# Performance work log

Measured on AMD Instinct MI355X. Metric: run time of the kernel, lower is better.

The kernel has to match this reference:

```python
import jax, jax.numpy as jnp
import numpy as np

FREQ_NUM = 3
MAX_STEP = 4
PERIODS = np.array([24.0, 7.0, 365.0], dtype=np.float32)  # ceil(sups - infs)
INFS = np.array([0.0, 0.0, 0.0], dtype=np.float32)
BS, H, W, L, D = 128, 56, 56, 64, 128
Z_DIM = 3 * H * W + L * D + D            # 17728
EMB_DIM = 2 * FREQ_NUM                   # sin/cos per frequency
IN_DIM = Z_DIM + 2 * EMB_DIM             # 17740
HID = 4096
N_POI, N_USER = 5000, 1000


def setup_inputs() -> dict:
    key = jax.random.key(0)
    ks = jax.random.split(key, 10)
    sups = jnp.asarray(PERIODS)
    return {
        "input_freq": jax.random.uniform(ks[0], (BS, H, W), jnp.float32),
        "input_seq": jax.random.randint(ks[1], (BS, L), 0, N_POI),
        "uid": jax.random.randint(ks[2], (BS,), 0, N_USER),
        "cur_time": jax.random.uniform(ks[3], (BS, FREQ_NUM), jnp.float32) * sups,
        "tar_time": jax.random.uniform(ks[4], (BS, FREQ_NUM), jnp.float32) * sups,
        "fuse_embed": jax.random.normal(ks[5], (N_POI + N_USER, D), jnp.float32),
        "W1": jax.random.normal(ks[6], (IN_DIM, HID), jnp.float32) / np.sqrt(IN_DIM),
        "b1": jnp.zeros((HID,), jnp.float32),
        "W2": jax.random.normal(ks[7], (HID, Z_DIM), jnp.float32) / np.sqrt(HID),
        "b2": jnp.zeros((Z_DIM,), jnp.float32),
        "n_poi": N_POI,
    }


def _time_grid(cur_time, tar_time):
    # Per-sample linspace with periodic wraparound; snapshot t0_ after each
    # micro-step assignment (intended semantics of the torch loop).
    periods = jnp.asarray(PERIODS)
    frac = jnp.linspace(0.0, 1.0, MAX_STEP)  # [4]
    rows = []
    t_cur = cur_time
    for j in range(FREQ_NUM):
        s = cur_time[:, j]
        e = tar_time[:, j]
        wrap = s > e
        e_adj = jnp.where(wrap, e + periods[j], e)
        inter = s[:, None] + (e_adj - s)[:, None] * frac[None, :]  # [bs,4]
        inter = jnp.where(wrap[:, None], jnp.mod(inter, periods[j]), inter)
        for k in range(MAX_STEP):
            t_cur = t_cur.at[:, j].set(inter[:, k])
            rows.append(t_cur)
    return jnp.stack(rows, axis=0)  # [4*freq_num, bs, freq_num]


def _time_embedding(T):
    # sinusoidal embedding per frequency band
    phase = 2.0 * jnp.pi * (T - jnp.asarray(INFS)) / jnp.asarray(PERIODS)
    return jnp.concatenate([jnp.sin(phase), jnp.cos(phase)], axis=-1)  # [S,bs,2F]


def reference(input_freq, input_seq, uid, cur_time, tar_time, fuse_embed,
              W1, b1, W2, b2, n_poi):
    bs = input_freq.shape[0]
    A = jnp.tile(input_freq[:, None], (1, 3, 1, 1)).reshape(bs, -1)     # [bs,3HW]
    x = fuse_embed[input_seq].transpose(0, 2, 1).reshape(bs, -1)        # [bs,D*L]
    u = fuse_embed[n_poi + uid].reshape(bs, -1)                          # [bs,D]
    z0 = jnp.concatenate([A, x, u], axis=-1)                             # [bs,Z_DIM]

    T = _time_grid(cur_time, tar_time)
    emb = _time_embedding(T)                                             # [S,bs,2F]

    def step(z, te):
        t0e, t1e = te
        inp = jnp.concatenate([z, t0e, t1e], axis=-1)
        dz = jnp.tanh(inp @ W1 + b1) @ W2 + b2
        return z + dz, None

    z, _ = jax.lax.scan(step, z0, (emb[:-1], emb[1:]))
    return z
```

## Files before the change

### kernel.cpp

```cpp
#include <hip/hip_runtime.h>
#include <math.h>

typedef __bf16 bf16;
typedef __bf16 bf16x8 __attribute__((ext_vector_type(8)));
typedef float f32x4 __attribute__((ext_vector_type(4)));

#define ZDIM 17728
#define HIDN 4096
#define BSZ 128

__device__ __forceinline__ void gl_lds16(const bf16* g, bf16* l) {
  __builtin_amdgcn_global_load_lds(
      (const __attribute__((address_space(1))) unsigned int*)g,
      (__attribute__((address_space(3))) unsigned int*)l, 16, 0, 0);
}

__global__ void k_cast_transpose(const float* __restrict__ src, bf16* __restrict__ dst,
                                 int K, int N) {
  __shared__ float t[32][33];
  int tx = threadIdx.x, ty = threadIdx.y;
  int k0 = blockIdx.y * 32, n0 = blockIdx.x * 32;
#pragma unroll
  for (int i = 0; i < 32; i += 8)
    t[ty + i][tx] = src[(size_t)(k0 + ty + i) * N + (n0 + tx)];
  __syncthreads();
#pragma unroll
  for (int i = 0; i < 32; i += 8)
    dst[(size_t)(n0 + ty + i) * K + (k0 + tx)] = (bf16)t[tx][ty + i];
}

__global__ void k_build_z0(const float* __restrict__ input_freq, const int* __restrict__ seq,
                           const int* __restrict__ uid, const float* __restrict__ fuse,
                           const int* __restrict__ n_poi_p,
                           float* __restrict__ z, bf16* __restrict__ zb) {
  int n = blockIdx.x * 256 + threadIdx.x;
  int b = blockIdx.y;
  if (n >= ZDIM) return;
  float v;
  if (n < 9408) {
    v = input_freq[b * 3136 + (n % 3136)];
  } else if (n < 17600) {
    int m = n - 9408;
    int d = m >> 6, l = m & 63;
    v = fuse[(size_t)seq[b * 64 + l] * 128 + d];
  } else {
    int d = n - 17600;
    v = fuse[(size_t)(n_poi_p[0] + uid[b]) * 128 + d];
  }
  size_t idx = (size_t)b * ZDIM + n;
  z[idx] = v;
  zb[idx] = (bf16)v;
}

__global__ void k_build_emb(const float* __restrict__ cur, const float* __restrict__ tar,
                            float* __restrict__ E) {
  int b = threadIdx.x;
  const float P[3] = {24.0f, 7.0f, 365.0f};
  const float TWO_PI = 6.283185307179586f;
  float t[3];
  for (int c = 0; c < 3; ++c) t[c] = cur[b * 3 + c];
  int r = 0;
  for (int j = 0; j < 3; ++j) {
    float s = cur[b * 3 + j], e = tar[b * 3 + j];
    bool wrap = s > e;
    float ea = wrap ? (e + P[j]) : e;
    for (int k = 0; k < 4; ++k) {
      float frac = (float)k / 3.0f;
      float v = s + (ea - s) * frac;
      if (wrap) v = v - floorf(v / P[j]) * P[j];
      t[j] = v;
      for (int c = 0; c < 3; ++c) {
        float ph = TWO_PI * t[c] / P[c];
        E[(r * BSZ + b) * 6 + c] = sinf(ph);
        E[(r * BSZ + b) * 6 + 3 + c] = cosf(ph);
      }
      ++r;
    }
  }
}

__global__ __launch_bounds__(256, 2) void k_gemm1(const bf16* __restrict__ A,
                                                  const bf16* __restrict__ Bt,
                                                  float* __restrict__ P) {
  __shared__ __align__(16) bf16 As[128 * 32];
  __shared__ __align__(16) bf16 Bs[128 * 32];
  const int tid = threadIdx.x;
  const int w = tid >> 6, lane = tid & 63;
  const int q = lane >> 4, r = lane & 15;
  const int nt = blockIdx.x, kc = blockIdx.y;
  const int nsteps = (kc < 2) ? 70 : 69;
  const int kstart = kc * 69 + ((kc < 2) ? kc : 2);

  const int srow = lane >> 2, sslot = lane & 3;
  const int sg = sslot ^ ((srow >> 2) & 3);
  const int rA0 = (2 * w) * 16 + srow;
  const int rA1 = (2 * w + 1) * 16 + srow;
  long k0 = (long)kstart * 32;
  const bf16* pA0 = A + (size_t)rA0 * ZDIM + k0 + sg * 8;
  const bf16* pA1 = A + (size_t)rA1 * ZDIM + k0 + sg * 8;
  const bf16* pB0 = Bt + (size_t)(nt * 128 + rA0) * ZDIM + k0 + sg * 8;
  const bf16* pB1 = Bt + (size_t)(nt * 128 + rA1) * ZDIM + k0 + sg * 8;
  bf16* lA0 = &As[(2 * w) * 512];
  bf16* lA1 = &As[(2 * w + 1) * 512];
  bf16* lB0 = &Bs[(2 * w) * 512];
  bf16* lB1 = &Bs[(2 * w + 1) * 512];

  const int swr = (r >> 2) & 3;
  const int aoff = r * 32 + (q ^ swr) * 8;
  const int boff0 = (32 * w + r) * 32 + (q ^ swr) * 8;
  const int boff1 = boff0 + 512;

  f32x4 zero4 = {0.f, 0.f, 0.f, 0.f};
  f32x4 acc[8][2];
#pragma unroll
  for (int mb = 0; mb < 8; ++mb) { acc[mb][0] = zero4; acc[mb][1] = zero4; }

  for (int s = 0; s < nsteps; ++s) {
    gl_lds16(pA0, lA0); gl_lds16(pA1, lA1);
    gl_lds16(pB0, lB0); gl_lds16(pB1, lB1);
    pA0 += 32; pA1 += 32; pB0 += 32; pB1 += 32;
    __syncthreads();
    bf16x8 bfr0 = *(const bf16x8*)&Bs[boff0];
    bf16x8 bfr1 = *(const bf16x8*)&Bs[boff1];
#pragma unroll
    for (int mb = 0; mb < 8; ++mb) {
      bf16x8 afr = *(const bf16x8*)&As[mb * 512 + aoff];
      acc[mb][0] = __builtin_amdgcn_mfma_f32_16x16x32_bf16(afr, bfr0, acc[mb][0], 0, 0, 0);
      acc[mb][1] = __builtin_amdgcn_mfma_f32_16x16x32_bf16(afr, bfr1, acc[mb][1], 0, 0, 0);
    }
    __syncthreads();
  }

  float* Pk = P + (size_t)kc * (BSZ * HIDN);
#pragma unroll
  for (int i = 0; i < 2; ++i) {
    int n = nt * 128 + (2 * w + i) * 16 + r;
#pragma unroll
    for (int mb = 0; mb < 8; ++mb) {
#pragma unroll
      for (int reg = 0; reg < 4; ++reg) {
        int brow = mb * 16 + q * 4 + reg;
        Pk[(size_t)brow * HIDN + n] = acc[mb][i][reg];
      }
    }
  }
}

__global__ void k_epi1(const float* __restrict__ P, const float* __restrict__ b1,
                       const float* __restrict__ W1, const float* __restrict__ E,
                       int step, bf16* __restrict__ Hb) {
  int idx = blockIdx.x * 256 + threadIdx.x;
  int b = idx >> 12, n = idx & 4095;
  float s = b1[n];
#pragma unroll
  for (int c = 0; c < 8; ++c) s += P[((size_t)c * BSZ + b) * HIDN + n];
  const float* e0 = E + ((size_t)step * BSZ + b) * 6;
  const float* e1 = e0 + BSZ * 6;
#pragma unroll
  for (int j = 0; j < 6; ++j) {
    s += e0[j] * W1[(size_t)(ZDIM + j) * HIDN + n];
    s += e1[j] * W1[(size_t)(ZDIM + 6 + j) * HIDN + n];
  }
  Hb[idx] = (bf16)tanhf(s);
}

__global__ __launch_bounds__(256, 2) void k_gemm2(const bf16* __restrict__ A,
                                                  const bf16* __restrict__ Bt,
                                                  const float* __restrict__ b2,
                                                  float* __restrict__ z,
                                                  bf16* __restrict__ zb) {
  __shared__ __align__(16) bf16 As[128 * 32];
  __shared__ __align__(16) bf16 Bs[64 * 32];
  const int tid = threadIdx.x;
  const int w = tid >> 6, lane = tid & 63;
  const int q = lane >> 4, r = lane & 15;
  const int nt = blockIdx.x;

  const int srow = lane >> 2, sslot = lane & 3;
  const int sg = sslot ^ ((srow >> 2) & 3);
  const int rA0 = (2 * w) * 16 + srow;
  const int rA1 = (2 * w + 1) * 16 + srow;
  const int rB = w * 16 + srow;
  const bf16* pA0 = A + (size_t)rA0 * HIDN + sg * 8;
  const bf16* pA1 = A + (size_t)rA1 * HIDN + sg * 8;
  const bf16* pB = Bt + (size_t)(nt * 64 + rB) * HIDN + sg * 8;
  bf16* lA0 = &As[(2 * w) * 512];
  bf16* lA1 = &As[(2 * w + 1) * 512];
  bf16* lB = &Bs[w * 512];

  const int swr = (r >> 2) & 3;
  const int aoff = r * 32 + (q ^ swr) * 8;
  const int boff = (w * 16 + r) * 32 + (q ^ swr) * 8;

  f32x4 zero4 = {0.f, 0.f, 0.f, 0.f};
  f32x4 acc[8];
#pragma unroll
  for (int mb = 0; mb < 8; ++mb) acc[mb] = zero4;

  for (int s = 0; s < 128; ++s) {
    gl_lds16(pA0, lA0); gl_lds16(pA1, lA1); gl_lds16(pB, lB);
    pA0 += 32; pA1 += 32; pB += 32;
    __syncthreads();
    bf16x8 bfr = *(const bf16x8*)&Bs[boff];
#pragma unroll
    for (int mb = 0; mb < 8; ++mb) {
      bf16x8 afr = *(const bf16x8*)&As[mb * 512 + aoff];
      acc[mb] = __builtin_amdgcn_mfma_f32_16x16x32_bf16(afr, bfr, acc[mb], 0, 0, 0);
    }
    __syncthreads();
  }

  int n = nt * 64 + w * 16 + r;
  float bias = b2[n];
#pragma unroll
  for (int mb = 0; mb < 8; ++mb) {
#pragma unroll
    for (int reg = 0; reg < 4; ++reg) {
      int brow = mb * 16 + q * 4 + reg;
      size_t idx = (size_t)brow * ZDIM + n;
      float v = z[idx] + acc[mb][reg] + bias;
      z[idx] = v;
      zb[idx] = (bf16)v;
    }
  }
}

extern "C" void kernel_launch(void* const* d_in, const int* in_sizes, int n_in,
                              void* d_out, int out_size, void* d_ws, size_t ws_size,
                              hipStream_t stream) {
  const float* input_freq = (const float*)d_in[0];
  const int* seq = (const int*)d_in[1];
  const int* uid = (const int*)d_in[2];
  const float* cur = (const float*)d_in[3];
  const float* tar = (const float*)d_in[4];
  const float* fuse = (const float*)d_in[5];
  const float* W1 = (const float*)d_in[6];
  const float* b1 = (const float*)d_in[7];
  const float* W2 = (const float*)d_in[8];
  const float* b2 = (const float*)d_in[9];
  const int* n_poi = (const int*)d_in[10];
  float* z = (float*)d_out;

  char* ws = (char*)d_ws;
  bf16* W1t = (bf16*)ws;
  bf16* W2t = (bf16*)(ws + 145227776);
  bf16* Zb = (bf16*)(ws + 290455552);
  bf16* Hb = (bf16*)(ws + 294993920);
  float* P = (float*)(ws + 296042496);
  float* E = (float*)(ws + 312819712);

  k_cast_transpose<<<dim3(HIDN / 32, ZDIM / 32), dim3(32, 8), 0, stream>>>(W1, W1t, ZDIM, HIDN);
  k_cast_transpose<<<dim3(ZDIM / 32, HIDN / 32), dim3(32, 8), 0, stream>>>(W2, W2t, HIDN, ZDIM);
  k_build_z0<<<dim3(70, BSZ), 256, 0, stream>>>(input_freq, seq, uid, fuse, n_poi, z, Zb);
  k_build_emb<<<1, BSZ, 0, stream>>>(cur, tar, E);

  for (int s = 0; s < 11; ++s) {
    k_gemm1<<<dim3(32, 8), 256, 0, stream>>>(Zb, W1t, P);
    k_epi1<<<2048, 256, 0, stream>>>(P, b1, W1, E, s, Hb);
    k_gemm2<<<277, 256, 0, stream>>>(Hb, W2t, b2, z, Zb);
  }
}
```

Before: 2.547 ms.

## Increase split-K for both GEMMs and add reduction epilogue for second GEMM

Raises the first GEMM's K-split from 8 to 24 chunks and adds a 4-way K-split to the second GEMM. The second GEMM now writes fp32 partials, and a new epilogue kernel sums them, adds the bias and updates z and its bf16 copy. The goal is to give the MI355X's many CUs more blocks than the previous 256/277-block grids could, which left many CUs idle. The cost is extra global traffic for the partial buffers and one more launch per step. The weight cast-transpose now also uses 64-row tiles with packed 32-bit bf16 stores.

```diff
diff --git a/kernel.cpp b/kernel.cpp
--- a/kernel.cpp
+++ b/kernel.cpp
@@ -8,6 +8,8 @@
 #define ZDIM 17728
 #define HIDN 4096
 #define BSZ 128
+#define KC1 24
+#define KC2 4
 
 __device__ __forceinline__ void gl_lds16(const bf16* g, bf16* l) {
   __builtin_amdgcn_global_load_lds(
@@ -17,16 +19,21 @@
 
 __global__ void k_cast_transpose(const float* __restrict__ src, bf16* __restrict__ dst,
                                  int K, int N) {
-  __shared__ float t[32][33];
+  __shared__ float t[64][33];
   int tx = threadIdx.x, ty = threadIdx.y;
-  int k0 = blockIdx.y * 32, n0 = blockIdx.x * 32;
-#pragma unroll
-  for (int i = 0; i < 32; i += 8)
+  int n0 = blockIdx.x * 32, k0 = blockIdx.y * 64;
+#pragma unroll
+  for (int i = 0; i < 64; i += 8)
     t[ty + i][tx] = src[(size_t)(k0 + ty + i) * N + (n0 + tx)];
   __syncthreads();
 #pragma unroll
-  for (int i = 0; i < 32; i += 8)
-    dst[(size_t)(n0 + ty + i) * K + (k0 + tx)] = (bf16)t[tx][ty + i];
+  for (int i = 0; i < 32; i += 8) {
+    int nl = ty + i;
+    union { bf16 h[2]; unsigned u; } p;
+    p.h[0] = (bf16)t[2 * tx][nl];
+    p.h[1] = (bf16)t[2 * tx + 1][nl];
+    *(unsigned*)&dst[(size_t)(n0 + nl) * K + k0 + 2 * tx] = p.u;
+  }
 }
 
 __global__ void k_build_z0(const float* __restrict__ input_freq, const int* __restrict__ seq,
@@ -79,7 +86,7 @@
   }
 }
 
-__global__ __launch_bounds__(256, 2) void k_gemm1(const bf16* __restrict__ A,
+__global__ __launch_bounds__(256, 3) void k_gemm1(const bf16* __restrict__ A,
                                                   const bf16* __restrict__ Bt,
                                                   float* __restrict__ P) {
   __shared__ __align__(16) bf16 As[128 * 32];
@@ -88,8 +95,8 @@
   const int w = tid >> 6, lane = tid & 63;
   const int q = lane >> 4, r = lane & 15;
   const int nt = blockIdx.x, kc = blockIdx.y;
-  const int nsteps = (kc < 2) ? 70 : 69;
-  const int kstart = kc * 69 + ((kc < 2) ? kc : 2);
+  const int nsteps = 23 + (kc < 2 ? 1 : 0);
+  const int kstart = kc * 23 + (kc < 2 ? kc : 2);
 
   const int srow = lane >> 2, sslot = lane & 3;
   const int sg = sslot ^ ((srow >> 2) & 3);
@@ -153,7 +160,7 @@
   int b = idx >> 12, n = idx & 4095;
   float s = b1[n];
 #pragma unroll
-  for (int c = 0; c < 8; ++c) s += P[((size_t)c * BSZ + b) * HIDN + n];
+  for (int c = 0; c < KC1; ++c) s += P[((size_t)c * BSZ + b) * HIDN + n];
   const float* e0 = E + ((size_t)step * BSZ + b) * 6;
   const float* e1 = e0 + BSZ * 6;
 #pragma unroll
@@ -164,26 +171,26 @@
   Hb[idx] = (bf16)tanhf(s);
 }
 
-__global__ __launch_bounds__(256, 2) void k_gemm2(const bf16* __restrict__ A,
+__global__ __launch_bounds__(256, 4) void k_gemm2(const bf16* __restrict__ A,
                                                   const bf16* __restrict__ Bt,
-                                                  const float* __restrict__ b2,
-                                                  float* __restrict__ z,
-                                                  bf16* __restrict__ zb) {
+                                                  float* __restrict__ P2) {
   __shared__ __align__(16) bf16 As[128 * 32];
   __shared__ __align__(16) bf16 Bs[64 * 32];
   const int tid = threadIdx.x;
   const int w = tid >> 6, lane = tid & 63;
   const int q = lane >> 4, r = lane & 15;
   const int nt = blockIdx.x;
+  const int kc = blockIdx.y;
+  const long k0 = (long)kc * 32 * 32;
 
   const int srow = lane >> 2, sslot = lane & 3;
   const int sg = sslot ^ ((srow >> 2) & 3);
   const int rA0 = (2 * w) * 16 + srow;
   const int rA1 = (2 * w + 1) * 16 + srow;
   const int rB = w * 16 + srow;
-  const bf16* pA0 = A + (size_t)rA0 * HIDN + sg * 8;
-  const bf16* pA1 = A + (size_t)rA1 * HIDN + sg * 8;
-  const bf16* pB = Bt + (size_t)(nt * 64 + rB) * HIDN + sg * 8;
+  const bf16* pA0 = A + (size_t)rA0 * HIDN + k0 + sg * 8;
+  const bf16* pA1 = A + (size_t)rA1 * HIDN + k0 + sg * 8;
+  const bf16* pB = Bt + (size_t)(nt * 64 + rB) * HIDN + k0 + sg * 8;
   bf16* lA0 = &As[(2 * w) * 512];
   bf16* lA1 = &As[(2 * w + 1) * 512];
   bf16* lB = &Bs[w * 512];
@@ -197,7 +204,7 @@
 #pragma unroll
   for (int mb = 0; mb < 8; ++mb) acc[mb] = zero4;
 
-  for (int s = 0; s < 128; ++s) {
+  for (int s = 0; s < 32; ++s) {
     gl_lds16(pA0, lA0); gl_lds16(pA1, lA1); gl_lds16(pB, lB);
     pA0 += 32; pA1 += 32; pB += 32;
     __syncthreads();
@@ -210,19 +217,28 @@
     __syncthreads();
   }
 
+  float* Pk = P2 + (size_t)kc * (BSZ * ZDIM);
   int n = nt * 64 + w * 16 + r;
-  float bias = b2[n];
 #pragma unroll
   for (int mb = 0; mb < 8; ++mb) {
 #pragma unroll
     for (int reg = 0; reg < 4; ++reg) {
       int brow = mb * 16 + q * 4 + reg;
-      size_t idx = (size_t)brow * ZDIM + n;
-      float v = z[idx] + acc[mb][reg] + bias;
-      z[idx] = v;
-      zb[idx] = (bf16)v;
-    }
-  }
+      Pk[(size_t)brow * ZDIM + n] = acc[mb][reg];
+    }
+  }
+}
+
+__global__ void k_epi2(const float* __restrict__ P2, const float* __restrict__ b2,
+                       float* __restrict__ z, bf16* __restrict__ zb) {
+  int idx = blockIdx.x * 256 + threadIdx.x;
+  int n = idx % ZDIM;
+  float s = b2[n];
+#pragma unroll
+  for (int c = 0; c < KC2; ++c) s += P2[(size_t)c * (BSZ * ZDIM) + idx];
+  float v = z[idx] + s;
+  z[idx] = v;
+  zb[idx] = (bf16)v;
 }
 
 extern "C" void kernel_launch(void* const* d_in, const int* in_sizes, int n_in,
@@ -247,16 +263,18 @@
   bf16* Zb = (bf16*)(ws + 290455552);
   bf16* Hb = (bf16*)(ws + 294993920);
   float* P = (float*)(ws + 296042496);
-  float* E = (float*)(ws + 312819712);
-
-  k_cast_transpose<<<dim3(HIDN / 32, ZDIM / 32), dim3(32, 8), 0, stream>>>(W1, W1t, ZDIM, HIDN);
-  k_cast_transpose<<<dim3(ZDIM / 32, HIDN / 32), dim3(32, 8), 0, stream>>>(W2, W2t, HIDN, ZDIM);
+  float* P2 = (float*)(ws + 296042496 + 50331648);
+  float* E = (float*)(ws + 296042496 + 50331648 + 36306944);
+
+  k_cast_transpose<<<dim3(HIDN / 32, ZDIM / 64), dim3(32, 8), 0, stream>>>(W1, W1t, ZDIM, HIDN);
+  k_cast_transpose<<<dim3(ZDIM / 32, HIDN / 64), dim3(32, 8), 0, stream>>>(W2, W2t, HIDN, ZDIM);
   k_build_z0<<<dim3(70, BSZ), 256, 0, stream>>>(input_freq, seq, uid, fuse, n_poi, z, Zb);
   k_build_emb<<<1, BSZ, 0, stream>>>(cur, tar, E);
 
   for (int s = 0; s < 11; ++s) {
-    k_gemm1<<<dim3(32, 8), 256, 0, stream>>>(Zb, W1t, P);
+    k_gemm1<<<dim3(32, KC1), 256, 0, stream>>>(Zb, W1t, P);
     k_epi1<<<2048, 256, 0, stream>>>(P, b1, W1, E, s, Hb);
-    k_gemm2<<<277, 256, 0, stream>>>(Hb, W2t, b2, z, Zb);
-  }
-}
+    k_gemm2<<<dim3(277, KC2), 256, 0, stream>>>(Hb, W2t, P2);
+    k_epi2<<<8864, 256, 0, stream>>>(P2, b2, z, Zb);
+  }
+}
```

After: 2.141 ms. 16.0% less time.
